# Optimization experiments

Measured on AMD Instinct MI355X. Metric: run time of the kernel, lower is better.

Reference implementation:

```python
import jax, jax.numpy as jnp
import numpy as np

N_ROWS = 8192
EMBED_DIM = 256


def setup_inputs() -> dict:
    key = jax.random.key(0)
    k1, k2, k3, k4, k5 = jax.random.split(key, 5)
    M = jax.random.normal(k1, (N_ROWS, EMBED_DIM), dtype=jnp.float32)
    N = jax.random.normal(k2, (N_ROWS, EMBED_DIM), dtype=jnp.float32)
    # gate_w: nn.Linear(embed_dim, 1) -> weight [1, d], bias [1]; gate_b extra scalar param [1]
    Wg = jax.random.normal(k3, (1, EMBED_DIM), dtype=jnp.float32) * 0.06
    bg = jax.random.normal(k4, (1,), dtype=jnp.float32) * 0.1
    gate_b = jax.random.normal(k5, (1,), dtype=jnp.float32) * 0.1
    return {"M": M, "N": N, "Wg": Wg, "bg": bg, "gate_b": gate_b, "iseval": 0}


def reference(M, N, Wg, bg, gate_b, iseval):
    # mt: [n, n] cross-similarity scores
    mt = jnp.matmul(N, M.T)
    if not iseval:
        # training branch: zero out the diagonal (mt - diag(diag(mt)))
        n = mt.shape[0]
        idx = jnp.arange(n)
        mt = mt.at[idx, idx].set(0.0)
    else:
        # eval branch: zero out the first row
        mt = mt.at[0].set(0.0)
    attn_weight = jax.nn.softmax(mt, axis=-1)          # [n, n]
    out_attn = jnp.matmul(attn_weight, M)              # [n, d]
    gate = jax.nn.sigmoid(jnp.matmul(out_attn, Wg.T) + bg + gate_b)  # [n, 1]
    boosted = out_attn * gate + N * (1.0 - gate)       # [n, d]
    return boosted[:, None, None, :]                   # [n, 1, 1, d]
```

## Files before the change

kernel.cpp:

```cpp
#include <hip/hip_runtime.h>


constexpr int EMBED = 256;
constexpr int BQ = 64;
constexpr int BJ = 32;
constexpr int NT = 256;

constexpr int SS_OFF = 0;
constexpr int PH_OFF = 18432;
constexpr int MS_OFF = 23552;
constexpr int LS_OFF = 23808;
constexpr int AS_OFF = 24064;
constexpr int LDS_SZ = 24320;

typedef _Float16 half8 __attribute__((ext_vector_type(8)));
typedef float f32x4 __attribute__((ext_vector_type(4)));
typedef short short8v __attribute__((ext_vector_type(8)));

static __device__ __forceinline__ f32x4 mfma16(half8 a, half8 b, f32x4 c) {
    return __builtin_amdgcn_mfma_f32_16x16x32_f16(a, b, c, 0, 0, 0);
}
static __device__ __forceinline__ short f2h(float x) {
    return (short)__builtin_bit_cast(unsigned short, (_Float16)x);
}

__global__ void prep(const float* __restrict__ M,
                     short* __restrict__ MhG, short* __restrict__ MtG) {
    __shared__ float L[16 * 260];
    const int r0 = blockIdx.x * 16;
    const int t = threadIdx.x;
    const int pj = t >> 4, pc = (t & 15) * 16;
    {
        const float* src = M + (size_t)(r0 + pj) * EMBED + pc;
        float4 v[4];
        #pragma unroll
        for (int i = 0; i < 4; ++i) v[i] = ((const float4*)src)[i];
        short* hd = MhG + (size_t)(r0 + pj) * EMBED + pc;
        #pragma unroll
        for (int i = 0; i < 2; ++i) {
            float4 a = v[2 * i], b = v[2 * i + 1];
            short8v h;
            h[0]=f2h(a.x); h[1]=f2h(a.y); h[2]=f2h(a.z); h[3]=f2h(a.w);
            h[4]=f2h(b.x); h[5]=f2h(b.y); h[6]=f2h(b.z); h[7]=f2h(b.w);
            *(short8v*)(hd + 8 * i) = h;
        }
        #pragma unroll
        for (int i = 0; i < 4; ++i)
            *(float4*)(L + pj * 260 + pc + 4 * i) = v[i];
    }
    __syncthreads();
    {
        const int d = t;
        const int tile = r0 >> 5, jh = (r0 >> 4) & 1;
        short* dst = MtG + (size_t)tile * (BJ * EMBED) + d * BJ + jh * 16;
        #pragma unroll
        for (int g2 = 0; g2 < 2; ++g2) {
            short8v w;
            #pragma unroll
            for (int e = 0; e < 8; ++e) w[e] = f2h(L[(g2 * 8 + e) * 260 + d]);
            *(short8v*)(dst + g2 * 8) = w;
        }
    }
}

__launch_bounds__(NT, 2)
__global__ void attn(const short* __restrict__ MhG, const short* __restrict__ MtG,
                     const float* __restrict__ Ng, const int* __restrict__ iseval_p,
                     float* __restrict__ O0out, short* __restrict__ Ofp,
                     float* __restrict__ MLm, float* __restrict__ MLl, int n)
{
    __shared__ __align__(16) char smem[LDS_SZ];
    float* MS = (float*)(smem + MS_OFF);
    float* LS = (float*)(smem + LS_OFF);
    float* AS = (float*)(smem + AS_OFF);

    const int t = threadIdx.x, lane = t & 63, wave = t >> 6;
    const int quad = lane >> 4, mn = lane & 15;
    const int bid = blockIdx.x;
    const int s  = (bid & 7) >> 1;
    const int qb = ((bid >> 3) << 1) | (bid & 1);
    const int q0 = qb * BQ;
    const int jbase = s * (n >> 2);
    const int jb32 = jbase / BJ;
    const int ntiles = (n >> 2) / BJ;
    const int iseval = *iseval_p;
    const int jt = wave & 1, kh = wave >> 1;
    const int dq = wave;
    const int sq = t >> 2, sh = t & 3;

    if (t < BQ) { MS[t] = -1e30f; LS[t] = 0.f; }

    half8 Qf[4][4];
    #pragma unroll
    for (int qi = 0; qi < 4; ++qi) {
        const float* np = Ng + (size_t)(q0 + qi * 16 + mn) * EMBED;
        #pragma unroll
        for (int kk = 0; kk < 4; ++kk) {
            const float* p = np + (kh * 4 + kk) * 32 + quad * 8;
            float4 a = *(const float4*)p, b = *(const float4*)(p + 4);
            half8 h;
            h[0]=(_Float16)a.x; h[1]=(_Float16)a.y; h[2]=(_Float16)a.z; h[3]=(_Float16)a.w;
            h[4]=(_Float16)b.x; h[5]=(_Float16)b.y; h[6]=(_Float16)b.z; h[7]=(_Float16)b.w;
            Qf[qi][kk] = h;
        }
    }

    f32x4 O[4][4];
    #pragma unroll
    for (int qi = 0; qi < 4; ++qi)
        #pragma unroll
        for (int dt = 0; dt < 4; ++dt) O[qi][dt] = (f32x4){0.f, 0.f, 0.f, 0.f};

    const short* mhb0 = MhG + (size_t)(jbase + jt * 16 + mn) * EMBED + kh * 128 + quad * 8;
    half8 Bc[4], Bn[4], Mtf[4];
    #pragma unroll
    for (int kk = 0; kk < 4; ++kk) Bc[kk] = *(const half8*)(mhb0 + kk * 32);

    __syncthreads();

    for (int tile = 0; tile < ntiles; ++tile) {
        const int j0g = jbase + tile * BJ;

        {
            f32x4 a0 = (f32x4){0,0,0,0}, a1 = (f32x4){0,0,0,0};
            f32x4 a2 = (f32x4){0,0,0,0}, a3 = (f32x4){0,0,0,0};
            #pragma unroll
            for (int kk = 0; kk < 4; ++kk) {
                half8 bf = Bc[kk];
                a0 = mfma16(Qf[0][kk], bf, a0);
                a1 = mfma16(Qf[1][kk], bf, a1);
                a2 = mfma16(Qf[2][kk], bf, a2);
                a3 = mfma16(Qf[3][kk], bf, a3);
            }
            float* ssp = (float*)(smem + SS_OFF) + kh * 2304;
            #pragma unroll
            for (int r = 0; r < 4; ++r) {
                ssp[(0  + quad * 4 + r) * 36 + jt * 16 + mn] = a0[r];
                ssp[(16 + quad * 4 + r) * 36 + jt * 16 + mn] = a1[r];
                ssp[(32 + quad * 4 + r) * 36 + jt * 16 + mn] = a2[r];
                ssp[(48 + quad * 4 + r) * 36 + jt * 16 + mn] = a3[r];
            }
        }
        __syncthreads();

        if (tile + 1 < ntiles) {
            const short* nb = mhb0 + (size_t)(tile + 1) * (BJ * EMBED);
            #pragma unroll
            for (int kk = 0; kk < 4; ++kk) Bn[kk] = *(const half8*)(nb + kk * 32);
        }
        {
            const short* mtb = MtG + (size_t)(jb32 + tile) * (BJ * EMBED);
            #pragma unroll
            for (int dt = 0; dt < 4; ++dt)
                Mtf[dt] = *(const half8*)(mtb + (dq * 64 + dt * 16 + mn) * BJ + quad * 8);
        }

        {
            const float* p0 = (const float*)(smem + SS_OFF) + sq * 36 + 8 * sh;
            float4 sa = *(const float4*)p0;
            float4 sb = *(const float4*)(p0 + 4);
            float4 sc = *(const float4*)(p0 + 2304);
            float4 sd = *(const float4*)(p0 + 2308);
            float sv[8] = {sa.x + sc.x, sa.y + sc.y, sa.z + sc.z, sa.w + sc.w,
                           sb.x + sd.x, sb.y + sd.y, sb.z + sd.z, sb.w + sd.w};
            const int qg = q0 + sq;
            if (iseval) {
                if (qg == 0) {
                    #pragma unroll
                    for (int i = 0; i < 8; ++i) sv[i] = 0.f;
                }
            } else {
                int dj = qg - j0g - 8 * sh;
                #pragma unroll
                for (int i = 0; i < 8; ++i) if (dj == i) sv[i] = 0.f;
            }
            float mx = sv[0];
            #pragma unroll
            for (int i = 1; i < 8; ++i) mx = fmaxf(mx, sv[i]);
            mx = fmaxf(mx, __shfl_xor(mx, 1));
            mx = fmaxf(mx, __shfl_xor(mx, 2));
            float m_old = MS[sq];
            float m_new = fmaxf(m_old, mx);
            float alpha = __expf(m_old - m_new);
            float p[8], ps = 0.f;
            #pragma unroll
            for (int i = 0; i < 8; ++i) { p[i] = __expf(sv[i] - m_new); ps += p[i]; }
            ps += __shfl_xor(ps, 1);
            ps += __shfl_xor(ps, 2);
            if (sh == 0) {
                MS[sq] = m_new;
                AS[sq] = alpha;
                LS[sq] = LS[sq] * alpha + ps;
            }
            half8 ph;
            #pragma unroll
            for (int i = 0; i < 8; ++i) ph[i] = (_Float16)p[i];
            *(half8*)(smem + PH_OFF + sq * 80 + sh * 16) = ph;
        }
        __syncthreads();

        #pragma unroll
        for (int qi = 0; qi < 4; ++qi) {
            half8 pf = *(const half8*)(smem + PH_OFF + (qi * 16 + mn) * 80 + quad * 16);
            f32x4 al = *(const f32x4*)((const float*)(smem + AS_OFF) + qi * 16 + quad * 4);
            #pragma unroll
            for (int dt = 0; dt < 4; ++dt) {
                f32x4 o = O[qi][dt];
                o[0] *= al[0]; o[1] *= al[1]; o[2] *= al[2]; o[3] *= al[3];
                O[qi][dt] = mfma16(pf, Mtf[dt], o);
            }
        }
        #pragma unroll
        for (int kk = 0; kk < 4; ++kk) Bc[kk] = Bn[kk];
    }

    if (s == 0) {
        #pragma unroll
        for (int qi = 0; qi < 4; ++qi)
            #pragma unroll
            for (int dt = 0; dt < 4; ++dt) {
                int col = dq * 64 + dt * 16 + mn;
                #pragma unroll
                for (int r = 0; r < 4; ++r)
                    O0out[(size_t)(q0 + qi * 16 + quad * 4 + r) * EMBED + col] = O[qi][dt][r];
            }
    } else {
        short* dst = Ofp + (size_t)(s - 1) * n * EMBED;
        #pragma unroll
        for (int qi = 0; qi < 4; ++qi)
            #pragma unroll
            for (int dt = 0; dt < 4; ++dt) {
                int col = dq * 64 + dt * 16 + mn;
                #pragma unroll
                for (int r = 0; r < 4; ++r)
                    dst[(size_t)(q0 + qi * 16 + quad * 4 + r) * EMBED + col] = f2h(O[qi][dt][r]);
            }
    }
    if (t < BQ) {
        MLm[s * n + q0 + t] = MS[t];
        MLl[s * n + q0 + t] = LS[t];
    }
}

__global__ void combine4(const float* __restrict__ O0, const short* __restrict__ Ofp,
                         const float* __restrict__ MLm, const float* __restrict__ MLl,
                         const float* __restrict__ Ng, const float* __restrict__ Wg,
                         const float* __restrict__ bg, const float* __restrict__ gb,
                         float* __restrict__ out, int n)
{
    const int t = threadIdx.x;
    const int row = blockIdx.x * 16 + (t >> 4);
    const int c = t & 15;
    float ms[4], ls[4];
    #pragma unroll
    for (int k = 0; k < 4; ++k) { ms[k] = MLm[k * n + row]; ls[k] = MLl[k * n + row]; }
    float m = fmaxf(fmaxf(ms[0], ms[1]), fmaxf(ms[2], ms[3]));
    float w[4], lsum = 0.f;
    #pragma unroll
    for (int k = 0; k < 4; ++k) { w[k] = __expf(ms[k] - m); lsum += w[k] * ls[k]; }
    float linv = 1.f / lsum;

    float acc[16];
    {
        const float4* o0 = (const float4*)(O0 + (size_t)row * EMBED + c * 16);
        #pragma unroll
        for (int i = 0; i < 4; ++i) {
            float4 v = o0[i];
            acc[4*i+0] = w[0] * v.x; acc[4*i+1] = w[0] * v.y;
            acc[4*i+2] = w[0] * v.z; acc[4*i+3] = w[0] * v.w;
        }
    }
    #pragma unroll
    for (int k = 1; k < 4; ++k) {
        const short* op = Ofp + (size_t)(k - 1) * n * EMBED + (size_t)row * EMBED + c * 16;
        half8 a = *(const half8*)op, b = *(const half8*)(op + 8);
        #pragma unroll
        for (int i = 0; i < 8; ++i) {
            acc[i]     += w[k] * (float)a[i];
            acc[8 + i] += w[k] * (float)b[i];
        }
    }
    float dot = 0.f;
    #pragma unroll
    for (int i = 0; i < 16; ++i) { acc[i] *= linv; dot += acc[i] * Wg[c * 16 + i]; }
    dot += __shfl_xor(dot, 1);
    dot += __shfl_xor(dot, 2);
    dot += __shfl_xor(dot, 4);
    dot += __shfl_xor(dot, 8);
    float g = 1.f / (1.f + __expf(-(dot + bg[0] + gb[0])));
    const float4* n4 = (const float4*)(Ng + (size_t)row * EMBED + c * 16);
    float4* o4 = (float4*)(out + (size_t)row * EMBED + c * 16);
    #pragma unroll
    for (int i = 0; i < 4; ++i) {
        float4 nn = n4[i];
        float4 res;
        res.x = acc[4*i+0] * g + nn.x * (1.f - g);
        res.y = acc[4*i+1] * g + nn.y * (1.f - g);
        res.z = acc[4*i+2] * g + nn.z * (1.f - g);
        res.w = acc[4*i+3] * g + nn.w * (1.f - g);
        o4[i] = res;
    }
}

extern "C" void kernel_launch(void* const* d_in, const int* in_sizes, int n_in,
                              void* d_out, int out_size, void* d_ws, size_t ws_size,
                              hipStream_t stream) {
    const float* M      = (const float*)d_in[0];
    const float* N      = (const float*)d_in[1];
    const float* Wgp    = (const float*)d_in[2];
    const float* bgp    = (const float*)d_in[3];
    const float* gbp    = (const float*)d_in[4];
    const int*   iseval = (const int*)d_in[5];
    float* out = (float*)d_out;

    int n = in_sizes[0] / EMBED;
    short* MhG = (short*)d_ws;
    short* MtG = MhG + (size_t)n * EMBED;
    short* Ofp = MtG + (size_t)n * EMBED;
    float* MLm = (float*)(Ofp + (size_t)3 * n * EMBED);
    float* MLl = MLm + 4 * n;

    hipLaunchKernelGGL(prep, dim3(n / 16), dim3(NT), 0, stream, M, MhG, MtG);
    hipLaunchKernelGGL(attn, dim3((n / BQ) * 4), dim3(NT), 0, stream,
                       MhG, MtG, N, iseval, out, Ofp, MLm, MLl, n);
    hipLaunchKernelGGL(combine4, dim3(n / 16), dim3(NT), 0, stream,
                       out, Ofp, MLm, MLl, N, Wgp, bgp, gbp, out, n);
}
```

Before: 187.4 us.

## Software-pipeline score MFMA with softmax via double-buffered LDS, one barrier per tile

Restructures the attention loop so tile t's QK^T scores are computed and stored into one LDS buffer while the softmax and PV update for tile t-1 read the other buffer. Scores, probabilities and alpha are now double-buffered, which removes one of the two __syncthreads per tile and lets the score MFMAs overlap with the softmax. In exchange LDS use roughly doubles to about 48KB per block, which may limit occupancy at two blocks per CU, and the loop runs one extra prologue/epilogue iteration.

```diff
diff --git a/kernel.cpp b/kernel.cpp
--- a/kernel.cpp
+++ b/kernel.cpp
@@ -7,11 +7,14 @@
 constexpr int NT = 256;
 
 constexpr int SS_OFF = 0;
-constexpr int PH_OFF = 18432;
-constexpr int MS_OFF = 23552;
-constexpr int LS_OFF = 23808;
-constexpr int AS_OFF = 24064;
-constexpr int LDS_SZ = 24320;
+constexpr int SS_BUF = 18432;
+constexpr int PH_OFF = 36864;
+constexpr int PH_BUF = 5120;
+constexpr int MS_OFF = 47104;
+constexpr int LS_OFF = 47360;
+constexpr int AS_OFF = 47616;
+constexpr int AS_BUF = 256;
+constexpr int LDS_SZ = 48128;
 
 typedef _Float16 half8 __attribute__((ext_vector_type(8)));
 typedef float f32x4 __attribute__((ext_vector_type(4)));
@@ -72,7 +75,6 @@
     __shared__ __align__(16) char smem[LDS_SZ];
     float* MS = (float*)(smem + MS_OFF);
     float* LS = (float*)(smem + LS_OFF);
-    float* AS = (float*)(smem + AS_OFF);
 
     const int t = threadIdx.x, lane = t & 63, wave = t >> 6;
     const int quad = lane >> 4, mn = lane & 15;
@@ -116,12 +118,18 @@
     #pragma unroll
     for (int kk = 0; kk < 4; ++kk) Bc[kk] = *(const half8*)(mhb0 + kk * 32);
 
-    __syncthreads();
-
-    for (int tile = 0; tile < ntiles; ++tile) {
-        const int j0g = jbase + tile * BJ;
-
-        {
+    for (int tt = 0; tt <= ntiles; ++tt) {
+        const int bw = tt & 1;
+        const int br = bw ^ 1;
+
+        if (tt > 0) {
+            const short* mtb = MtG + (size_t)(jb32 + (tt - 1)) * (BJ * EMBED);
+            #pragma unroll
+            for (int dt = 0; dt < 4; ++dt)
+                Mtf[dt] = *(const half8*)(mtb + (dq * 64 + dt * 16 + mn) * BJ + quad * 8);
+        }
+
+        if (tt < ntiles) {
             f32x4 a0 = (f32x4){0,0,0,0}, a1 = (f32x4){0,0,0,0};
             f32x4 a2 = (f32x4){0,0,0,0}, a3 = (f32x4){0,0,0,0};
             #pragma unroll
@@ -132,7 +140,7 @@
                 a2 = mfma16(Qf[2][kk], bf, a2);
                 a3 = mfma16(Qf[3][kk], bf, a3);
             }
-            float* ssp = (float*)(smem + SS_OFF) + kh * 2304;
+            float* ssp = (float*)(smem + SS_OFF + bw * SS_BUF) + kh * 2304;
             #pragma unroll
             for (int r = 0; r < 4; ++r) {
                 ssp[(0  + quad * 4 + r) * 36 + jt * 16 + mn] = a0[r];
@@ -141,22 +149,16 @@
                 ssp[(48 + quad * 4 + r) * 36 + jt * 16 + mn] = a3[r];
             }
         }
-        __syncthreads();
-
-        if (tile + 1 < ntiles) {
-            const short* nb = mhb0 + (size_t)(tile + 1) * (BJ * EMBED);
+
+        if (tt + 1 < ntiles) {
+            const short* nb = mhb0 + (size_t)(tt + 1) * (BJ * EMBED);
             #pragma unroll
             for (int kk = 0; kk < 4; ++kk) Bn[kk] = *(const half8*)(nb + kk * 32);
         }
-        {
-            const short* mtb = MtG + (size_t)(jb32 + tile) * (BJ * EMBED);
-            #pragma unroll
-            for (int dt = 0; dt < 4; ++dt)
-                Mtf[dt] = *(const half8*)(mtb + (dq * 64 + dt * 16 + mn) * BJ + quad * 8);
-        }
-
-        {
-            const float* p0 = (const float*)(smem + SS_OFF) + sq * 36 + 8 * sh;
+
+        if (tt > 0) {
+            const int j0g = jbase + (tt - 1) * BJ;
+            const float* p0 = (const float*)(smem + SS_OFF + br * SS_BUF) + sq * 36 + 8 * sh;
             float4 sa = *(const float4*)p0;
             float4 sb = *(const float4*)(p0 + 4);
             float4 sc = *(const float4*)(p0 + 2304);
@@ -189,27 +191,31 @@
             ps += __shfl_xor(ps, 2);
             if (sh == 0) {
                 MS[sq] = m_new;
-                AS[sq] = alpha;
+                ((float*)(smem + AS_OFF + br * AS_BUF))[sq] = alpha;
                 LS[sq] = LS[sq] * alpha + ps;
             }
             half8 ph;
             #pragma unroll
             for (int i = 0; i < 8; ++i) ph[i] = (_Float16)p[i];
-            *(half8*)(smem + PH_OFF + sq * 80 + sh * 16) = ph;
-        }
+            *(half8*)(smem + PH_OFF + br * PH_BUF + sq * 80 + sh * 16) = ph;
+        }
+
         __syncthreads();
 
-        #pragma unroll
-        for (int qi = 0; qi < 4; ++qi) {
-            half8 pf = *(const half8*)(smem + PH_OFF + (qi * 16 + mn) * 80 + quad * 16);
-            f32x4 al = *(const f32x4*)((const float*)(smem + AS_OFF) + qi * 16 + quad * 4);
-            #pragma unroll
-            for (int dt = 0; dt < 4; ++dt) {
-                f32x4 o = O[qi][dt];
-                o[0] *= al[0]; o[1] *= al[1]; o[2] *= al[2]; o[3] *= al[3];
-                O[qi][dt] = mfma16(pf, Mtf[dt], o);
-            }
-        }
+        if (tt > 0) {
+            #pragma unroll
+            for (int qi = 0; qi < 4; ++qi) {
+                half8 pf = *(const half8*)(smem + PH_OFF + br * PH_BUF + (qi * 16 + mn) * 80 + quad * 16);
+                f32x4 al = *(const f32x4*)((const float*)(smem + AS_OFF + br * AS_BUF) + qi * 16 + quad * 4);
+                #pragma unroll
+                for (int dt = 0; dt < 4; ++dt) {
+                    f32x4 o = O[qi][dt];
+                    o[0] *= al[0]; o[1] *= al[1]; o[2] *= al[2]; o[3] *= al[3];
+                    O[qi][dt] = mfma16(pf, Mtf[dt], o);
+                }
+            }
+        }
+
         #pragma unroll
         for (int kk = 0; kk < 4; ++kk) Bc[kk] = Bn[kk];
     }
```

Result: no change. 185.3 us (-1.2%).
